# Performance work log

Measured on AMD Instinct MI355X. Metric: run time of the kernel, lower is better.

## Reference

```python
import jax, jax.numpy as jnp
import numpy as np

BATCH, SEQ, D_MODEL, K_SIZE = 2, 4096, 2048, 3


def setup_inputs() -> dict:
    key = jax.random.key(0)
    k1, k2, k3, k4 = jax.random.split(key, 4)
    s = 1.0 / np.sqrt(D_MODEL)
    x = jax.random.normal(k1, (BATCH, SEQ, D_MODEL), dtype=jnp.float32)
    w1 = jax.random.normal(k2, (3 * D_MODEL, D_MODEL), dtype=jnp.float32) * s
    w2 = jax.random.normal(k3, (D_MODEL, D_MODEL), dtype=jnp.float32) * s
    conv_w = jax.random.normal(k4, (D_MODEL, 1, K_SIZE), dtype=jnp.float32) * 0.5
    return {"x": x, "w1": w1, "w2": w2, "conv_w": conv_w}


def _causal_depthwise_conv(u, conv_w):
    # u: [B, D, S]; conv_w: [D, 1, K] (torch Conv1d weight layout, groups=D)
    k = conv_w.shape[-1]
    return jax.lax.conv_general_dilated(
        u, conv_w,
        window_strides=(1,),
        padding=[(k - 1, 0)],  # left pad = causal; matches pad=k-1 then [..., :seq_len]
        feature_group_count=u.shape[1],
        dimension_numbers=("NCH", "OIH", "NCH"),
    )


def reference(x, w1, w2, conv_w):
    # x: [B, S, D]
    BCx = jnp.einsum("bsd,ed->bse", x, w1)           # [B, S, 3D]
    Bg, Cg, Xg = jnp.split(BCx, 3, axis=-1)           # each [B, S, D]
    u = (Bg * Xg).transpose(0, 2, 1)                  # [B, D, S]
    conv_out = _causal_depthwise_conv(u, conv_w)      # [B, D, S]
    gated = Cg * conv_out.transpose(0, 2, 1)          # [B, S, D]
    return jnp.einsum("bsd,ed->bse", gated, w2)       # [B, S, D]
```

## Files before the change

kernel.cpp:

```cpp
#include <hip/hip_runtime.h>
#include <stdint.h>

#define BATCH 2
#define SEQ   4096
#define DM    2048
#define MT    (BATCH*SEQ)
#define N1    (3*DM)
#define STRIP 16

typedef __attribute__((ext_vector_type(8))) __bf16 bf16x8;
typedef __attribute__((ext_vector_type(4))) float  f32x4;
typedef __attribute__((ext_vector_type(8))) unsigned short ushort8v;
typedef __attribute__((ext_vector_type(4))) unsigned short ushort4v;

__device__ inline unsigned short f2bf(float f) {
    uint32_t u = __float_as_uint(f);
    u += 0x7FFFu + ((u >> 16) & 1u);
    return (unsigned short)(u >> 16);
}
__device__ inline float bf2f(unsigned short h) {
    return __uint_as_float(((uint32_t)h) << 16);
}

__global__ void cvt_f32_bf16(const float* __restrict__ src,
                             unsigned short* __restrict__ dst, int n) {
    int i = (blockIdx.x * blockDim.x + threadIdx.x) * 4;
    const int stride = gridDim.x * blockDim.x * 4;
    for (; i < n; i += stride) {
        const float4 v = *(const float4*)(src + i);
        ushort4v o;
        o[0] = f2bf(v.x); o[1] = f2bf(v.y); o[2] = f2bf(v.z); o[3] = f2bf(v.w);
        *(ushort4v*)(dst + i) = o;
    }
}

__device__ inline void async_copy16(const void* g, void* l) {
    __builtin_amdgcn_global_load_lds(
        (const __attribute__((address_space(1))) void*)g,
        (__attribute__((address_space(3))) void*)l,
        16, 0, 0);
}


#define MFMA_(d, a, b) d = __builtin_amdgcn_mfma_f32_16x16x32_bf16(a, b, d, 0, 0, 0)

#define QUAD(MH, NH, BQ) do { \
  MFMA_(acc[(MH)*4+0][(NH)*2+0], af[0][0], BQ[0][0]); MFMA_(acc[(MH)*4+0][(NH)*2+0], af[0][1], BQ[0][1]); \
  MFMA_(acc[(MH)*4+0][(NH)*2+1], af[0][0], BQ[1][0]); MFMA_(acc[(MH)*4+0][(NH)*2+1], af[0][1], BQ[1][1]); \
  MFMA_(acc[(MH)*4+1][(NH)*2+0], af[1][0], BQ[0][0]); MFMA_(acc[(MH)*4+1][(NH)*2+0], af[1][1], BQ[0][1]); \
  MFMA_(acc[(MH)*4+1][(NH)*2+1], af[1][0], BQ[1][0]); MFMA_(acc[(MH)*4+1][(NH)*2+1], af[1][1], BQ[1][1]); \
  MFMA_(acc[(MH)*4+2][(NH)*2+0], af[2][0], BQ[0][0]); MFMA_(acc[(MH)*4+2][(NH)*2+0], af[2][1], BQ[0][1]); \
  MFMA_(acc[(MH)*4+2][(NH)*2+1], af[2][0], BQ[1][0]); MFMA_(acc[(MH)*4+2][(NH)*2+1], af[2][1], BQ[1][1]); \
  MFMA_(acc[(MH)*4+3][(NH)*2+0], af[3][0], BQ[0][0]); MFMA_(acc[(MH)*4+3][(NH)*2+0], af[3][1], BQ[0][1]); \
  MFMA_(acc[(MH)*4+3][(NH)*2+1], af[3][0], BQ[1][0]); MFMA_(acc[(MH)*4+3][(NH)*2+1], af[3][1], BQ[1][1]); \
} while (0)

template <bool OUT_BF16>
__global__ __launch_bounds__(512)
void gemm256(const unsigned short* __restrict__ A,
             const unsigned short* __restrict__ B,
             void* __restrict__ Cout, int M, int N, int K) {
    __shared__ __attribute__((aligned(16))) char lds[131072];
    const int tid  = threadIdx.x;
    const int wave = tid >> 6;
    const int lane = tid & 63;
    const int wr = wave >> 2, wc = wave & 3;
    const int l16 = lane & 15, lh = lane >> 4;
    const int NT = K >> 6;

    const int nx = gridDim.x;
    int flat = blockIdx.y * nx + blockIdx.x;
    const int cpx = (nx * gridDim.y) >> 3;
    flat = (flat & 7) * cpx + (flat >> 3);
    const int blockN = (flat % nx) << 8;
    const int blockM = (flat / nx) << 8;

    const int swze = ((((lane & 7) << 4) ^ ((lane >> 3) << 4)) >> 1);
    const int sr   = (wave << 3) + (lane >> 3);
    const unsigned short* Ab = A + (size_t)blockM * K;
    const unsigned short* Bb = B + (size_t)blockN * K;
    const size_t a00 = (size_t)(sr      ) * K + swze;
    const size_t a01 = (size_t)(sr +  64) * K + swze;
    const size_t a10 = (size_t)(sr + 128) * K + swze;
    const size_t a11 = (size_t)(sr + 192) * K + swze;
    const int bsr = ((wave >> 2) << 6) + ((wave & 3) << 3) + (lane >> 3);
    const size_t b00 = (size_t)(bsr      ) * K + swze;
    const size_t b01 = (size_t)(bsr + 128) * K + swze;
    const size_t b10 = (size_t)(bsr +  32) * K + swze;
    const size_t b11 = (size_t)(bsr + 160) * K + swze;
    const int ldsw = wave << 10;

#define STG_A(BUF, U, K0) do { \
    async_copy16(Ab + a##U##0 + (K0), lds + (BUF) + (U)*16384 + ldsw); \
    async_copy16(Ab + a##U##1 + (K0), lds + (BUF) + (U)*16384 + 8192 + ldsw); } while (0)
#define STG_B(BUF, NH, K0) do { \
    async_copy16(Bb + b##NH##0 + (K0), lds + (BUF) + 32768 + (NH)*16384 + ldsw); \
    async_copy16(Bb + b##NH##1 + (K0), lds + (BUF) + 32768 + (NH)*16384 + 8192 + ldsw); } while (0)

    const int rdswz = (l16 & 7) << 4;
    const int ac0 = ((lh << 4)      ) ^ rdswz;
    const int ac1 = (64 + (lh << 4)) ^ rdswz;
    const int aRB = wr * 16384 + l16 * 128;
    const int bRB = 32768 + (wc * 32 + l16) * 128;

#define LDA_(BUF, I, C) (*(const bf16x8*)(lds + (BUF) + aRB + (I)*2048 + (C)))
#define LDB_(BUF, J, C) (*(const bf16x8*)(lds + (BUF) + bRB + ((J)>>1)*16384 + ((J)&1)*2048 + (C)))

    f32x4 acc[8][4] = {};
    bf16x8 af[4][2], bq0[2][2], bq1[2][2];

    STG_B(0, 0, 0); STG_B(0, 1, 0); STG_A(0, 0, 0); STG_A(0, 1, 0);
    if (NT > 1) {
        STG_B(65536, 0, 64); STG_B(65536, 1, 64); STG_A(65536, 0, 64);
        asm volatile("s_waitcnt vmcnt(6)" ::: "memory");
    } else {
        asm volatile("s_waitcnt vmcnt(0)" ::: "memory");
    }
    __builtin_amdgcn_s_barrier();

#define ITER(CUR, NXT, T) do { \
     \
    af[0][0]=LDA_(CUR,0,ac0); af[0][1]=LDA_(CUR,0,ac1); \
    af[1][0]=LDA_(CUR,1,ac0); af[1][1]=LDA_(CUR,1,ac1); \
    af[2][0]=LDA_(CUR,2,ac0); af[2][1]=LDA_(CUR,2,ac1); \
    af[3][0]=LDA_(CUR,3,ac0); af[3][1]=LDA_(CUR,3,ac1); \
    bq0[0][0]=LDB_(CUR,0,ac0); bq0[0][1]=LDB_(CUR,0,ac1); \
    bq0[1][0]=LDB_(CUR,1,ac0); bq0[1][1]=LDB_(CUR,1,ac1); \
    if ((T) + 1 < NT) STG_A(NXT, 1, ((T)+1)*64); \
    __builtin_amdgcn_s_barrier(); \
    __builtin_amdgcn_s_setprio(1); \
    QUAD(0, 0, bq0); \
    __builtin_amdgcn_s_setprio(0); \
    __builtin_amdgcn_s_barrier(); \
     \
    bq1[0][0]=LDB_(CUR,2,ac0); bq1[0][1]=LDB_(CUR,2,ac1); \
    bq1[1][0]=LDB_(CUR,3,ac0); bq1[1][1]=LDB_(CUR,3,ac1); \
    if ((T) + 2 < NT) STG_B(CUR, 0, ((T)+2)*64); \
    __builtin_amdgcn_s_barrier(); \
    __builtin_amdgcn_s_setprio(1); \
    QUAD(0, 1, bq1); \
    __builtin_amdgcn_s_setprio(0); \
    __builtin_amdgcn_s_barrier(); \
     \
    af[0][0]=LDA_(CUR,4,ac0); af[0][1]=LDA_(CUR,4,ac1); \
    af[1][0]=LDA_(CUR,5,ac0); af[1][1]=LDA_(CUR,5,ac1); \
    af[2][0]=LDA_(CUR,6,ac0); af[2][1]=LDA_(CUR,6,ac1); \
    af[3][0]=LDA_(CUR,7,ac0); af[3][1]=LDA_(CUR,7,ac1); \
    if ((T) + 2 < NT) STG_B(CUR, 1, ((T)+2)*64); \
    __builtin_amdgcn_s_barrier(); \
    __builtin_amdgcn_s_setprio(1); \
    QUAD(1, 1, bq1); \
    __builtin_amdgcn_s_setprio(0); \
    __builtin_amdgcn_s_barrier(); \
     \
    if ((T) + 2 < NT) STG_A(CUR, 0, ((T)+2)*64); \
    __builtin_amdgcn_s_barrier(); \
    __builtin_amdgcn_s_setprio(1); \
    QUAD(1, 0, bq0); \
    __builtin_amdgcn_s_setprio(0); \
    if ((T) + 2 < NT)      { asm volatile("s_waitcnt vmcnt(6)" ::: "memory"); } \
    else if ((T) + 1 < NT) { asm volatile("s_waitcnt vmcnt(0)" ::: "memory"); } \
    __builtin_amdgcn_s_barrier(); \
} while (0)

    for (int t = 0; t < NT; t += 2) {
        ITER(0, 65536, t);
        ITER(65536, 0, t + 1);
    }

    const int orow = blockM + wr * 128 + (lh << 2);
    const int ocol = blockN + wc * 64 + l16;
    #pragma unroll
    for (int i = 0; i < 8; ++i) {
        #pragma unroll
        for (int j = 0; j < 4; ++j) {
            #pragma unroll
            for (int r = 0; r < 4; ++r) {
                const int row = orow + i * 16 + r;
                const int col = ocol + j * 16;
                if constexpr (OUT_BF16)
                    ((unsigned short*)Cout)[(size_t)row * N + col] = f2bf(acc[i][j][r]);
                else
                    ((float*)Cout)[(size_t)row * N + col] = acc[i][j][r];
            }
        }
    }
#undef ITER
#undef LDA_
#undef LDB_
#undef STG_A
#undef STG_B
}

__global__ void conv_gate_kernel(const unsigned short* __restrict__ BCx,
                                 const float* __restrict__ cw,
                                 unsigned short* __restrict__ gated) {
    const int tid = threadIdx.x;
    const int d0  = tid * 8;
    const int nstrips = SEQ / STRIP;
    const int b   = blockIdx.x / nstrips;
    const int s0  = (blockIdx.x % nstrips) * STRIP;

    float w0[8], w1c[8], w2c[8];
    #pragma unroll
    for (int c = 0; c < 8; ++c) {
        w0[c]  = cw[(d0 + c) * 3 + 0];
        w1c[c] = cw[(d0 + c) * 3 + 1];
        w2c[c] = cw[(d0 + c) * 3 + 2];
    }

    float um1[8], um2[8];
    if (s0 > 0) {
        const unsigned short* r2 = BCx + (size_t)(b * SEQ + s0 - 2) * N1;
        const unsigned short* r1 = BCx + (size_t)(b * SEQ + s0 - 1) * N1;
        ushort8v bg2 = *(const ushort8v*)(r2 + d0);
        ushort8v xg2 = *(const ushort8v*)(r2 + 2 * DM + d0);
        ushort8v bg1 = *(const ushort8v*)(r1 + d0);
        ushort8v xg1 = *(const ushort8v*)(r1 + 2 * DM + d0);
        #pragma unroll
        for (int c = 0; c < 8; ++c) {
            um2[c] = bf2f(bg2[c]) * bf2f(xg2[c]);
            um1[c] = bf2f(bg1[c]) * bf2f(xg1[c]);
        }
    } else {
        #pragma unroll
        for (int c = 0; c < 8; ++c) { um2[c] = 0.f; um1[c] = 0.f; }
    }

    for (int s = s0; s < s0 + STRIP; ++s) {
        const size_t m = (size_t)b * SEQ + s;
        const unsigned short* rp = BCx + m * N1;
        ushort8v bg = *(const ushort8v*)(rp + d0);
        ushort8v cg = *(const ushort8v*)(rp + DM + d0);
        ushort8v xg = *(const ushort8v*)(rp + 2 * DM + d0);
        ushort8v og;
        #pragma unroll
        for (int c = 0; c < 8; ++c) {
            const float u    = bf2f(bg[c]) * bf2f(xg[c]);
            const float conv = w0[c] * um2[c] + w1c[c] * um1[c] + w2c[c] * u;
            const float g    = bf2f(cg[c]) * conv;
            um2[c] = um1[c];
            um1[c] = u;
            og[c]  = f2bf(g);
        }
        *(ushort8v*)(gated + m * DM + d0) = og;
    }
}

extern "C" void kernel_launch(void* const* d_in, const int* in_sizes, int n_in,
                              void* d_out, int out_size, void* d_ws, size_t ws_size,
                              hipStream_t stream) {
    const float* x   = (const float*)d_in[0];
    const float* w1  = (const float*)d_in[1];
    const float* w2  = (const float*)d_in[2];
    const float* cw  = (const float*)d_in[3];
    float* out = (float*)d_out;

    char* ws = (char*)d_ws;
    unsigned short* x_bf   = (unsigned short*)ws;
    unsigned short* w1_bf  = x_bf  + (size_t)MT * DM;
    unsigned short* w2_bf  = w1_bf + (size_t)N1 * DM;
    unsigned short* bcx_bf = w2_bf + (size_t)DM * DM;
    unsigned short* g_bf   = bcx_bf + (size_t)MT * N1;

    cvt_f32_bf16<<<2048, 256, 0, stream>>>(x,  x_bf,  MT * DM);
    cvt_f32_bf16<<<1024, 256, 0, stream>>>(w1, w1_bf, N1 * DM);
    cvt_f32_bf16<<<512,  256, 0, stream>>>(w2, w2_bf, DM * DM);

    gemm256<true><<<dim3(N1 / 256, MT / 256), 512, 0, stream>>>(
        x_bf, w1_bf, bcx_bf, MT, N1, DM);

    conv_gate_kernel<<<BATCH * (SEQ / STRIP), 256, 0, stream>>>(bcx_bf, cw, g_bf);

    gemm256<false><<<dim3(DM / 256, MT / 256), 512, 0, stream>>>(
        g_bf, w2_bf, out, MT, DM, DM);
}
```

Measured before the change: 313.1 us.

## Restructure GEMM main loop into 8-phase ping-pong with register double-buffered fragments

Splits each K-iteration of the bf16 GEMM into eight smaller MFMA phases of 8 instructions each. A-fragments are double-buffered in registers (afP/afQ) so the LDS reads for the next phase, including the first fragments of the next K tile, are issued while the current MFMAs run. Global-to-LDS staging is redistributed and the vmcnt waits are adjusted to match. The aim is to hide LDS read latency behind matrix math, at the cost of more barriers, more live registers, and subtle correctness risk in the buffer reuse ordering.

```diff
diff --git a/kernel.cpp b/kernel.cpp
--- a/kernel.cpp
+++ b/kernel.cpp
@@ -44,15 +44,11 @@
 
 #define MFMA_(d, a, b) d = __builtin_amdgcn_mfma_f32_16x16x32_bf16(a, b, d, 0, 0, 0)
 
-#define QUAD(MH, NH, BQ) do { \
-  MFMA_(acc[(MH)*4+0][(NH)*2+0], af[0][0], BQ[0][0]); MFMA_(acc[(MH)*4+0][(NH)*2+0], af[0][1], BQ[0][1]); \
-  MFMA_(acc[(MH)*4+0][(NH)*2+1], af[0][0], BQ[1][0]); MFMA_(acc[(MH)*4+0][(NH)*2+1], af[0][1], BQ[1][1]); \
-  MFMA_(acc[(MH)*4+1][(NH)*2+0], af[1][0], BQ[0][0]); MFMA_(acc[(MH)*4+1][(NH)*2+0], af[1][1], BQ[0][1]); \
-  MFMA_(acc[(MH)*4+1][(NH)*2+1], af[1][0], BQ[1][0]); MFMA_(acc[(MH)*4+1][(NH)*2+1], af[1][1], BQ[1][1]); \
-  MFMA_(acc[(MH)*4+2][(NH)*2+0], af[2][0], BQ[0][0]); MFMA_(acc[(MH)*4+2][(NH)*2+0], af[2][1], BQ[0][1]); \
-  MFMA_(acc[(MH)*4+2][(NH)*2+1], af[2][0], BQ[1][0]); MFMA_(acc[(MH)*4+2][(NH)*2+1], af[2][1], BQ[1][1]); \
-  MFMA_(acc[(MH)*4+3][(NH)*2+0], af[3][0], BQ[0][0]); MFMA_(acc[(MH)*4+3][(NH)*2+0], af[3][1], BQ[0][1]); \
-  MFMA_(acc[(MH)*4+3][(NH)*2+1], af[3][0], BQ[1][0]); MFMA_(acc[(MH)*4+3][(NH)*2+1], af[3][1], BQ[1][1]); \
+#define M8(K2, NH, AH, BQ) do { \
+  MFMA_(acc[(K2)+0][(NH)*2+0], AH[0][0], BQ[0][0]); MFMA_(acc[(K2)+0][(NH)*2+0], AH[0][1], BQ[0][1]); \
+  MFMA_(acc[(K2)+0][(NH)*2+1], AH[0][0], BQ[1][0]); MFMA_(acc[(K2)+0][(NH)*2+1], AH[0][1], BQ[1][1]); \
+  MFMA_(acc[(K2)+1][(NH)*2+0], AH[1][0], BQ[0][0]); MFMA_(acc[(K2)+1][(NH)*2+0], AH[1][1], BQ[0][1]); \
+  MFMA_(acc[(K2)+1][(NH)*2+1], AH[1][0], BQ[1][0]); MFMA_(acc[(K2)+1][(NH)*2+1], AH[1][1], BQ[1][1]); \
 } while (0)
 
 template <bool OUT_BF16>
@@ -106,61 +102,63 @@
 #define LDA_(BUF, I, C) (*(const bf16x8*)(lds + (BUF) + aRB + (I)*2048 + (C)))
 #define LDB_(BUF, J, C) (*(const bf16x8*)(lds + (BUF) + bRB + ((J)>>1)*16384 + ((J)&1)*2048 + (C)))
 
+#define RD_A(DST, BUF, HI) do { \
+    DST[0][0]=LDA_(BUF,2*(HI)  ,ac0); DST[0][1]=LDA_(BUF,2*(HI)  ,ac1); \
+    DST[1][0]=LDA_(BUF,2*(HI)+1,ac0); DST[1][1]=LDA_(BUF,2*(HI)+1,ac1); } while (0)
+#define RD_B(DST, BUF, NH) do { \
+    DST[0][0]=LDB_(BUF,2*(NH)  ,ac0); DST[0][1]=LDB_(BUF,2*(NH)  ,ac1); \
+    DST[1][0]=LDB_(BUF,2*(NH)+1,ac0); DST[1][1]=LDB_(BUF,2*(NH)+1,ac1); } while (0)
+
     f32x4 acc[8][4] = {};
-    bf16x8 af[4][2], bq0[2][2], bq1[2][2];
+    bf16x8 afP[2][2], afQ[2][2], bq0[2][2], bq1[2][2];
 
     STG_B(0, 0, 0); STG_B(0, 1, 0); STG_A(0, 0, 0); STG_A(0, 1, 0);
-    if (NT > 1) {
-        STG_B(65536, 0, 64); STG_B(65536, 1, 64); STG_A(65536, 0, 64);
-        asm volatile("s_waitcnt vmcnt(6)" ::: "memory");
-    } else {
-        asm volatile("s_waitcnt vmcnt(0)" ::: "memory");
-    }
+    STG_B(65536, 0, 64); STG_B(65536, 1, 64);
+    STG_A(65536, 0, 64); STG_A(65536, 1, 64);
+    asm volatile("s_waitcnt vmcnt(8)" ::: "memory");
     __builtin_amdgcn_s_barrier();
+    RD_B(bq0, 0, 0);
+    RD_A(afP, 0, 0);
+
+#define SP1 __builtin_amdgcn_s_setprio(1)
+#define SP0 __builtin_amdgcn_s_setprio(0)
 
 #define ITER(CUR, NXT, T) do { \
      \
-    af[0][0]=LDA_(CUR,0,ac0); af[0][1]=LDA_(CUR,0,ac1); \
-    af[1][0]=LDA_(CUR,1,ac0); af[1][1]=LDA_(CUR,1,ac1); \
-    af[2][0]=LDA_(CUR,2,ac0); af[2][1]=LDA_(CUR,2,ac1); \
-    af[3][0]=LDA_(CUR,3,ac0); af[3][1]=LDA_(CUR,3,ac1); \
-    bq0[0][0]=LDB_(CUR,0,ac0); bq0[0][1]=LDB_(CUR,0,ac1); \
-    bq0[1][0]=LDB_(CUR,1,ac0); bq0[1][1]=LDB_(CUR,1,ac1); \
-    if ((T) + 1 < NT) STG_A(NXT, 1, ((T)+1)*64); \
-    __builtin_amdgcn_s_barrier(); \
-    __builtin_amdgcn_s_setprio(1); \
-    QUAD(0, 0, bq0); \
-    __builtin_amdgcn_s_setprio(0); \
-    __builtin_amdgcn_s_barrier(); \
-     \
-    bq1[0][0]=LDB_(CUR,2,ac0); bq1[0][1]=LDB_(CUR,2,ac1); \
-    bq1[1][0]=LDB_(CUR,3,ac0); bq1[1][1]=LDB_(CUR,3,ac1); \
+    __builtin_amdgcn_s_barrier(); \
+    RD_B(bq1, CUR, 1); \
+    RD_A(afQ, CUR, 1); \
+    SP1; M8(0, 0, afP, bq0); SP0; \
+     \
+    __builtin_amdgcn_s_barrier(); \
     if ((T) + 2 < NT) STG_B(CUR, 0, ((T)+2)*64); \
-    __builtin_amdgcn_s_barrier(); \
-    __builtin_amdgcn_s_setprio(1); \
-    QUAD(0, 1, bq1); \
-    __builtin_amdgcn_s_setprio(0); \
-    __builtin_amdgcn_s_barrier(); \
-     \
-    af[0][0]=LDA_(CUR,4,ac0); af[0][1]=LDA_(CUR,4,ac1); \
-    af[1][0]=LDA_(CUR,5,ac0); af[1][1]=LDA_(CUR,5,ac1); \
-    af[2][0]=LDA_(CUR,6,ac0); af[2][1]=LDA_(CUR,6,ac1); \
-    af[3][0]=LDA_(CUR,7,ac0); af[3][1]=LDA_(CUR,7,ac1); \
+    SP1; M8(0, 1, afP, bq1); SP0; \
+     \
+    __builtin_amdgcn_s_barrier(); \
+    RD_A(afP, CUR, 2); \
+    SP1; M8(2, 0, afQ, bq0); SP0; \
+     \
+    __builtin_amdgcn_s_barrier(); \
     if ((T) + 2 < NT) STG_B(CUR, 1, ((T)+2)*64); \
-    __builtin_amdgcn_s_barrier(); \
-    __builtin_amdgcn_s_setprio(1); \
-    QUAD(1, 1, bq1); \
-    __builtin_amdgcn_s_setprio(0); \
-    __builtin_amdgcn_s_barrier(); \
-     \
-    if ((T) + 2 < NT) STG_A(CUR, 0, ((T)+2)*64); \
-    __builtin_amdgcn_s_barrier(); \
-    __builtin_amdgcn_s_setprio(1); \
-    QUAD(1, 0, bq0); \
-    __builtin_amdgcn_s_setprio(0); \
-    if ((T) + 2 < NT)      { asm volatile("s_waitcnt vmcnt(6)" ::: "memory"); } \
+    SP1; M8(2, 1, afQ, bq1); SP0; \
+     \
+    __builtin_amdgcn_s_barrier(); \
+    RD_A(afQ, CUR, 3); \
+    SP1; M8(4, 0, afP, bq0); SP0; \
+     \
+    __builtin_amdgcn_s_barrier(); \
+    SP1; M8(4, 1, afP, bq1); SP0; \
+    if ((T) + 2 < NT)      { asm volatile("s_waitcnt vmcnt(4)" ::: "memory"); } \
     else if ((T) + 1 < NT) { asm volatile("s_waitcnt vmcnt(0)" ::: "memory"); } \
-    __builtin_amdgcn_s_barrier(); \
+     \
+    __builtin_amdgcn_s_barrier(); \
+    if ((T) + 1 < NT) RD_A(afP, NXT, 0); \
+    SP1; M8(6, 0, afQ, bq0); SP0; \
+     \
+    __builtin_amdgcn_s_barrier(); \
+    if ((T) + 2 < NT) { STG_A(CUR, 0, ((T)+2)*64); STG_A(CUR, 1, ((T)+2)*64); } \
+    if ((T) + 1 < NT) RD_B(bq0, NXT, 0); \
+    SP1; M8(6, 1, afQ, bq1); SP0; \
 } while (0)
 
     for (int t = 0; t < NT; t += 2) {
@@ -186,6 +184,8 @@
         }
     }
 #undef ITER
+#undef RD_A
+#undef RD_B
 #undef LDA_
 #undef LDB_
 #undef STG_A
```

Measured after the change: 308.5 us. About the same (-1.5%).
